# Performance work log

Measured on AMD Instinct MI355X. Metric: run time of the kernel, lower is better.

The kernel has to match this reference:

```python
import jax, jax.numpy as jnp
import numpy as np

B, S, D = 2, 2048, 1024
H = 16
HD = D // H  # 64


def setup_inputs() -> dict:
    key = jax.random.key(0)
    ks = jax.random.split(key, 6)
    sc = 1.0 / np.sqrt(D)
    x = jax.random.normal(ks[0], (B, S, D), dtype=jnp.float32)
    Wq = jax.random.normal(ks[1], (D, D), dtype=jnp.float32) * sc
    Wk = jax.random.normal(ks[2], (D, D), dtype=jnp.float32) * sc
    Wv = jax.random.normal(ks[3], (D, D), dtype=jnp.float32) * sc
    Wo = jax.random.normal(ks[4], (D, D), dtype=jnp.float32) * sc
    bo = jax.random.normal(ks[5], (D,), dtype=jnp.float32) * 0.01
    return {"x": x, "Wq": Wq, "Wk": Wk, "Wv": Wv, "Wo": Wo, "bo": bo}


def reference(x, Wq, Wk, Wv, Wo, bo):
    # projections: [B,S,D] -> [B,H,S,HD]
    def split_heads(t):
        return t.reshape(B, S, H, HD).transpose(0, 2, 1, 3)

    q = split_heads(x @ Wq)
    k = split_heads(x @ Wk)
    v = split_heads(x @ Wv)

    # naive full score matrix [B,H,S,S], masked causal, scaled softmax
    scores = jnp.einsum("bhqd,bhkd->bhqk", q, k)
    causal = jnp.tril(jnp.ones((S, S), dtype=bool))  # True = keep
    scores = jnp.where(causal, scores, -jnp.inf)
    attn = jax.nn.softmax(scores / np.sqrt(HD), axis=-1)

    ctx = jnp.einsum("bhqk,bhkd->bhqd", attn, v)  # [B,H,S,HD]
    ctx = ctx.transpose(0, 2, 1, 3).reshape(B, S, D)
    return ctx @ Wo + bo
```

## Files before the change

kernel.cpp:

```cpp
#include <hip/hip_runtime.h>

#define BB 2
#define SS 2048
#define DD 1024
#define HH 16
#define HD 64
#define MM (BB*SS)

typedef __bf16 bf16x8 __attribute__((ext_vector_type(8)));
typedef short  s16x4  __attribute__((ext_vector_type(4)));
typedef float  f32x4  __attribute__((ext_vector_type(4)));

#ifndef __has_builtin
#define __has_builtin(x) 0
#endif

__device__ __forceinline__ unsigned short f2bf(float f) {
    unsigned int u = __float_as_uint(f);
    u = (u + 0x7fffu + ((u >> 16) & 1u)) >> 16;
    return (unsigned short)u;
}
__device__ __forceinline__ unsigned int pack2(float a, float b) {
    return (unsigned int)f2bf(a) | ((unsigned int)f2bf(b) << 16);
}
__device__ __forceinline__ unsigned int pack2_fast(float a, float b) {
#if __has_builtin(__builtin_amdgcn_perm)
    return __builtin_amdgcn_perm(__float_as_uint(b) + 0x8000u,
                                 __float_as_uint(a) + 0x8000u, 0x07060302u);
#else
    return ((__float_as_uint(a) + 0x8000u) >> 16) |
           ((__float_as_uint(b) + 0x8000u) & 0xffff0000u);
#endif
}

__device__ __forceinline__ void gload_lds16(const unsigned short* g, unsigned short* l) {
    __builtin_amdgcn_global_load_lds(
        (const __attribute__((address_space(1))) void*)g,
        (__attribute__((address_space(3))) void*)l, 16, 0, 0);
}

__global__ __launch_bounds__(256) void cast_x_kernel(const float* __restrict__ x,
                                                     unsigned short* __restrict__ Xb) {
    int gid = blockIdx.x * 256 + threadIdx.x;
    int i = gid * 8;
    float4 a = *(const float4*)(x + i);
    float4 b = *(const float4*)(x + i + 4);
    uint4 o;
    o.x = pack2(a.x, a.y); o.y = pack2(a.z, a.w);
    o.z = pack2(b.x, b.y); o.w = pack2(b.z, b.w);
    ((uint4*)Xb)[gid] = o;
}

__global__ __launch_bounds__(256) void prep_w_kernel(const float* __restrict__ Wq,
                                                     const float* __restrict__ Wk,
                                                     const float* __restrict__ Wv,
                                                     const float* __restrict__ Wo,
                                                     unsigned short* __restrict__ Wqkvt,
                                                     unsigned short* __restrict__ Wot) {
    __shared__ float tile[32][33];
    int p = blockIdx.z;
    const float* src = (p == 0) ? Wq : (p == 1) ? Wk : (p == 2) ? Wv : Wo;
    unsigned short* dst = (p == 3) ? Wot : (Wqkvt + (size_t)p * DD * DD);
    int tx = threadIdx.x, ty = threadIdx.y;
    int n = blockIdx.x * 32 + tx;
#pragma unroll
    for (int i = 0; i < 4; ++i) {
        int k = blockIdx.y * 32 + ty + i * 8;
        tile[ty + i * 8][tx] = src[k * DD + n];
    }
    __syncthreads();
#pragma unroll
    for (int i = 0; i < 4; ++i) {
        int n2 = blockIdx.x * 32 + ty + i * 8;
        int k2 = blockIdx.y * 32 + tx;
        dst[n2 * DD + k2] = f2bf(tile[tx][ty + i * 8]);
    }
}

#define GEMM_K_LOOP(Aglob, Bglob)                                                 \
    __shared__ unsigned short smem[128 * 132];                                    \
    unsigned short (*As)[64]  = (unsigned short(*)[64])smem;                      \
    unsigned short (*Bs)[64]  = (unsigned short(*)[64])(smem + 128 * 64);         \
    unsigned short (*Es)[132] = (unsigned short(*)[132])smem;                     \
    const int n0 = blockIdx.x * 128, m0 = blockIdx.y * 128;                       \
    const int t = threadIdx.x;                                                    \
    const int wave = t >> 6, lane = t & 63;                                       \
    const int wm = wave >> 1, wn = wave & 1;                                      \
    const int l15 = lane & 15, quad = lane >> 4;                                  \
    const int lr = lane >> 3, lc = (lane & 7) * 8;                                \
    f32x4 acc[4][4];                                                              \
    _Pragma("unroll") for (int i = 0; i < 4; ++i)                                 \
        _Pragma("unroll") for (int j = 0; j < 4; ++j) acc[i][j] = f32x4{0,0,0,0}; \
    for (int kt = 0; kt < 16; ++kt) {                                             \
        if (kt) __syncthreads();                                                  \
        _Pragma("unroll") for (int i = 0; i < 4; ++i) {                           \
            int row = wave * 32 + i * 8;                                          \
            gload_lds16(Aglob + (size_t)(m0 + row + lr) * DD + kt * 64 + lc, &As[row][0]); \
            gload_lds16(Bglob + (size_t)(n0 + row + lr) * DD + kt * 64 + lc, &Bs[row][0]); \
        }                                                                         \
        __syncthreads();                                                          \
        _Pragma("unroll") for (int kh = 0; kh < 2; ++kh) {                        \
            bf16x8 af[4], bfr[4];                                                 \
            _Pragma("unroll") for (int s = 0; s < 4; ++s)                         \
                af[s] = *(const bf16x8*)&As[wm * 64 + s * 16 + l15][kh * 32 + quad * 8]; \
            _Pragma("unroll") for (int s = 0; s < 4; ++s)                         \
                bfr[s] = *(const bf16x8*)&Bs[wn * 64 + s * 16 + l15][kh * 32 + quad * 8]; \
            _Pragma("unroll") for (int i = 0; i < 4; ++i)                         \
                _Pragma("unroll") for (int j = 0; j < 4; ++j)                     \
                    acc[i][j] = __builtin_amdgcn_mfma_f32_16x16x32_bf16(af[i], bfr[j], acc[i][j], 0, 0, 0); \
        }                                                                         \
    }                                                                             \
    __syncthreads();

__global__ __launch_bounds__(256) void qkv_gemm_kernel(const unsigned short* __restrict__ Xb,
                                                       const unsigned short* __restrict__ Wt,
                                                       unsigned short* __restrict__ Qg,
                                                       unsigned short* __restrict__ Kg,
                                                       unsigned short* __restrict__ Vt) {
    GEMM_K_LOOP(Xb, Wt)
    const int p = n0 >> 10;
    const float qs = (p == 0) ? 0.18033688011112042f : 1.0f;
    if (p < 2) {
#pragma unroll
        for (int sm = 0; sm < 4; ++sm)
#pragma unroll
            for (int sn = 0; sn < 4; ++sn)
#pragma unroll
                for (int i = 0; i < 4; ++i)
                    Es[wm * 64 + sm * 16 + quad * 4 + i][wn * 64 + sn * 16 + l15] = f2bf(acc[sm][sn][i] * qs);
    } else {
#pragma unroll
        for (int sm = 0; sm < 4; ++sm)
#pragma unroll
            for (int sn = 0; sn < 4; ++sn)
#pragma unroll
                for (int i = 0; i < 4; ++i)
                    Es[wn * 64 + sn * 16 + l15][wm * 64 + sm * 16 + quad * 4 + i] = f2bf(acc[sm][sn][i]);
    }
    __syncthreads();
    const int h0 = (n0 & 1023) >> 6;
    if (p < 2) {
        unsigned short* dst0 = p ? Kg : Qg;
        int ml = t >> 1, seg = t & 1;
        int gm = m0 + ml, b = gm >> 11, s = gm & 2047;
        unsigned short* dptr = dst0 + ((size_t)(b * HH + h0 + seg) * SS + s) * HD;
#pragma unroll
        for (int j = 0; j < 8; ++j)
            *(uint4*)(dptr + j * 8) = *(const uint4*)&Es[ml][seg * 64 + j * 8];
    } else {
        int nl = t >> 1, mh = t & 1;
        int h = h0 + (nl >> 6), hd = nl & 63;
        int b = m0 >> 11, s0 = (m0 & 2047) + mh * 64;
        unsigned short* dptr = Vt + ((size_t)(b * HH + h) * HD + hd) * SS + s0;
#pragma unroll
        for (int j = 0; j < 8; ++j)
            *(uint4*)(dptr + j * 8) = *(const uint4*)&Es[nl][mh * 64 + j * 8];
    }
}

__global__ __launch_bounds__(256) void out_gemm_kernel(const unsigned short* __restrict__ Ctxb,
                                                       const unsigned short* __restrict__ Wot,
                                                       const float* __restrict__ bo,
                                                       float* __restrict__ out) {
    GEMM_K_LOOP(Ctxb, Wot)
    (void)Es;
#pragma unroll
    for (int sn = 0; sn < 4; ++sn) {
        int gn = n0 + wn * 64 + sn * 16 + l15;
        float bias = bo[gn];
#pragma unroll
        for (int sm = 0; sm < 4; ++sm)
#pragma unroll
            for (int i = 0; i < 4; ++i) {
                int gm = m0 + wm * 64 + sm * 16 + quad * 4 + i;
                out[(size_t)gm * DD + gn] = acc[sm][sn][i] + bias;
            }
    }
}

__global__ __launch_bounds__(256) void attn_kernel(const unsigned short* __restrict__ Qg,
                                                   const unsigned short* __restrict__ Kg,
                                                   const unsigned short* __restrict__ Vt,
                                                   unsigned short* __restrict__ Ctxb) {
    __shared__ unsigned short Ks[2][64][64];
    __shared__ unsigned short Vs[2][64][64];

    const int bh = blockIdx.x;
    const int qt = (int)gridDim.y - 1 - (int)blockIdx.y;
    const int t = threadIdx.x;
    const int wave = t >> 6, lane = t & 63;
    const int l15 = lane & 15, quad = lane >> 4;
    const int q0 = qt * 64;
    const int b = bh >> 4, h = bh & 15;

    const unsigned short* Qb = Qg + (size_t)bh * SS * HD;
    const unsigned short* Kb = Kg + (size_t)bh * SS * HD;
    const unsigned short* Vb = Vt + (size_t)bh * HD * SS;

    const int qrow = q0 + wave * 16 + l15;
    bf16x8 bq[2];
#pragma unroll
    for (int hh = 0; hh < 2; ++hh)
        bq[hh] = *(const bf16x8*)(Qb + (size_t)qrow * HD + hh * 32 + quad * 8);

    const int rloc = lane >> 3, pcl = lane & 7;
    const int csw = pcl ^ rloc;
    const unsigned short* ksrc[2];
    const unsigned short* vsrc[2];
#pragma unroll
    for (int j = 0; j < 2; ++j) {
        int row = (wave * 2 + j) * 8 + rloc;
        ksrc[j] = Kb + (size_t)row * HD + csw * 8;
        vsrc[j] = Vb + (size_t)row * SS + csw * 8;
    }

    f32x4 acc[4] = {f32x4{0,0,0,0}, f32x4{0,0,0,0}, f32x4{0,0,0,0}, f32x4{0,0,0,0}};
    float l = 0.f;
    const int nkt = qt + 1;

#pragma unroll
    for (int j = 0; j < 2; ++j) {
        gload_lds16(ksrc[j], &Ks[0][(wave * 2 + j) * 8][0]);
        gload_lds16(vsrc[j], &Vs[0][(wave * 2 + j) * 8][0]);
    }
    __syncthreads();

    for (int kt = 0; kt < nkt; ++kt) {
        const int buf = kt & 1;
        const int k0 = kt * 64;
        if (kt + 1 < nkt) {
            const int nb = buf ^ 1;
#pragma unroll
            for (int j = 0; j < 2; ++j) {
                gload_lds16(ksrc[j] + (size_t)(kt + 1) * 4096, &Ks[nb][(wave * 2 + j) * 8][0]);
                gload_lds16(vsrc[j] + (kt + 1) * 64,           &Vs[nb][(wave * 2 + j) * 8][0]);
            }
        }

        f32x4 St[4] = {f32x4{0,0,0,0}, f32x4{0,0,0,0}, f32x4{0,0,0,0}, f32x4{0,0,0,0}};
#pragma unroll
        for (int hh = 0; hh < 2; ++hh) {
            const int pcK = (hh * 4 + quad) ^ (l15 & 7);
            bf16x8 ak[4];
#pragma unroll
            for (int kb = 0; kb < 4; ++kb)
                ak[kb] = *(const bf16x8*)&Ks[buf][0][(kb * 16 + l15) * 64 + pcK * 8];
#pragma unroll
            for (int kb = 0; kb < 4; ++kb)
                St[kb] = __builtin_amdgcn_mfma_f32_16x16x32_bf16(ak[kb], bq[hh], St[kb], 0, 0, 0);
        }

        if (kt == qt) {
#pragma unroll
            for (int kb = 0; kb < 4; ++kb)
#pragma unroll
                for (int r = 0; r < 4; ++r)
                    if (k0 + kb * 16 + quad * 4 + r > qrow) St[kb][r] = -1e30f;
        }

        float lt = 0.f;
        s16x4 ap[4];
#pragma unroll
        for (int kb = 0; kb < 4; ++kb) {
            float e0 = __builtin_amdgcn_exp2f(St[kb][0]);
            float e1 = __builtin_amdgcn_exp2f(St[kb][1]);
            float e2 = __builtin_amdgcn_exp2f(St[kb][2]);
            float e3 = __builtin_amdgcn_exp2f(St[kb][3]);
            lt += (e0 + e1) + (e2 + e3);
            uint2 uu;
            uu.x = pack2_fast(e0, e1);
            uu.y = pack2_fast(e2, e3);
            ap[kb] = *(s16x4*)&uu;
        }
        lt += __shfl_xor(lt, 16, 64);
        lt += __shfl_xor(lt, 32, 64);
        l += lt;

#pragma unroll
        for (int kb = 0; kb < 4; ++kb) {
            s16x4 bv[4];
#pragma unroll
            for (int db = 0; db < 4; ++db) {
                const int pcV = (2 * kb + (quad >> 1)) ^ (l15 & 7);
                bv[db] = *(const s16x4*)&Vs[buf][0][(db * 16 + l15) * 64 + pcV * 8 + (quad & 1) * 4];
            }
#pragma unroll
            for (int db = 0; db < 4; ++db)
                acc[db] = __builtin_amdgcn_mfma_f32_16x16x16bf16_1k(ap[kb], bv[db], acc[db], 0, 0, 0);
        }

        if (kt + 1 < nkt) __syncthreads();
    }

    float linv = 1.0f / l;
#pragma unroll
    for (int r = 0; r < 4; ++r) {
        float ir = __shfl(linv, quad * 4 + r, 64);
        int gq = q0 + wave * 16 + quad * 4 + r;
        size_t base = ((size_t)(b * SS + gq)) * DD + h * HD;
#pragma unroll
        for (int db = 0; db < 4; ++db)
            Ctxb[base + db * 16 + l15] = f2bf(acc[db][r] * ir);
    }
}

extern "C" void kernel_launch(void* const* d_in, const int* in_sizes, int n_in,
                              void* d_out, int out_size, void* d_ws, size_t ws_size,
                              hipStream_t stream) {
    const float* x  = (const float*)d_in[0];
    const float* Wq = (const float*)d_in[1];
    const float* Wk = (const float*)d_in[2];
    const float* Wv = (const float*)d_in[3];
    const float* Wo = (const float*)d_in[4];
    const float* bo = (const float*)d_in[5];
    float* out = (float*)d_out;

    char* w = (char*)d_ws;
    unsigned short* Xb    = (unsigned short*)(w);
    unsigned short* Wqkvt = (unsigned short*)(w + (size_t)(8 << 20));
    unsigned short* Wot   = (unsigned short*)(w + (size_t)(14 << 20));
    unsigned short* Qg    = (unsigned short*)(w + (size_t)(16 << 20));
    unsigned short* Kg    = (unsigned short*)(w + (size_t)(24 << 20));
    unsigned short* Vt    = (unsigned short*)(w + (size_t)(32 << 20));
    unsigned short* Ctxb  = (unsigned short*)(w + (size_t)(40 << 20));

    cast_x_kernel<<<MM * DD / (256 * 8), 256, 0, stream>>>(x, Xb);
    prep_w_kernel<<<dim3(DD / 32, DD / 32, 4), dim3(32, 8), 0, stream>>>(Wq, Wk, Wv, Wo, Wqkvt, Wot);
    qkv_gemm_kernel<<<dim3(3 * DD / 128, MM / 128), 256, 0, stream>>>(Xb, Wqkvt, Qg, Kg, Vt);
    attn_kernel<<<dim3(BB * HH, SS / 64), 256, 0, stream>>>(Qg, Kg, Vt, Ctxb);
    out_gemm_kernel<<<dim3(DD / 128, MM / 128), 256, 0, stream>>>(Ctxb, Wot, bo, out);
}
```

Baseline: 186.5 us.

## Merge prep kernels and use 128-wide KV tiles in causal attention

Merges the x cast and weight transpose kernels into one launch that picks its job from the block index. The attention kernel now loads 128 keys per iteration (double-buffered K and V tiles in LDS with a new XOR swizzle) and processes them in 16-key chunks, skipping fully masked chunks on the final tile. The row-sum shuffle reduction moves out of the loop to the end. The goal is fewer barriers and loop iterations and one less kernel launch, at the cost of doubled LDS use, which may lower occupancy.

```diff
diff --git a/kernel.cpp b/kernel.cpp
--- a/kernel.cpp
+++ b/kernel.cpp
@@ -39,40 +39,45 @@
         (__attribute__((address_space(3))) void*)l, 16, 0, 0);
 }
 
-__global__ __launch_bounds__(256) void cast_x_kernel(const float* __restrict__ x,
-                                                     unsigned short* __restrict__ Xb) {
-    int gid = blockIdx.x * 256 + threadIdx.x;
-    int i = gid * 8;
-    float4 a = *(const float4*)(x + i);
-    float4 b = *(const float4*)(x + i + 4);
-    uint4 o;
-    o.x = pack2(a.x, a.y); o.y = pack2(a.z, a.w);
-    o.z = pack2(b.x, b.y); o.w = pack2(b.z, b.w);
-    ((uint4*)Xb)[gid] = o;
-}
-
-__global__ __launch_bounds__(256) void prep_w_kernel(const float* __restrict__ Wq,
-                                                     const float* __restrict__ Wk,
-                                                     const float* __restrict__ Wv,
-                                                     const float* __restrict__ Wo,
-                                                     unsigned short* __restrict__ Wqkvt,
-                                                     unsigned short* __restrict__ Wot) {
+__global__ __launch_bounds__(256) void prep_kernel(const float* __restrict__ x,
+                                                   const float* __restrict__ Wq,
+                                                   const float* __restrict__ Wk,
+                                                   const float* __restrict__ Wv,
+                                                   const float* __restrict__ Wo,
+                                                   unsigned short* __restrict__ Xb,
+                                                   unsigned short* __restrict__ Wqkvt,
+                                                   unsigned short* __restrict__ Wot) {
     __shared__ float tile[32][33];
-    int p = blockIdx.z;
+    const int bx = blockIdx.x;
+    const int t = threadIdx.x;
+    if (bx < 2048) {
+        int gid = bx * 256 + t;
+        int i = gid * 8;
+        float4 a = *(const float4*)(x + i);
+        float4 b = *(const float4*)(x + i + 4);
+        uint4 o;
+        o.x = pack2(a.x, a.y); o.y = pack2(a.z, a.w);
+        o.z = pack2(b.x, b.y); o.w = pack2(b.z, b.w);
+        ((uint4*)Xb)[gid] = o;
+        return;
+    }
+    int pb = bx - 2048;
+    int p = pb >> 10, rem = pb & 1023;
+    int bxx = rem & 31, byy = rem >> 5;
     const float* src = (p == 0) ? Wq : (p == 1) ? Wk : (p == 2) ? Wv : Wo;
     unsigned short* dst = (p == 3) ? Wot : (Wqkvt + (size_t)p * DD * DD);
-    int tx = threadIdx.x, ty = threadIdx.y;
-    int n = blockIdx.x * 32 + tx;
+    int tx = t & 31, ty = t >> 5;
+    int n = bxx * 32 + tx;
 #pragma unroll
     for (int i = 0; i < 4; ++i) {
-        int k = blockIdx.y * 32 + ty + i * 8;
+        int k = byy * 32 + ty + i * 8;
         tile[ty + i * 8][tx] = src[k * DD + n];
     }
     __syncthreads();
 #pragma unroll
     for (int i = 0; i < 4; ++i) {
-        int n2 = blockIdx.x * 32 + ty + i * 8;
-        int k2 = blockIdx.y * 32 + tx;
+        int n2 = bxx * 32 + ty + i * 8;
+        int k2 = byy * 32 + tx;
         dst[n2 * DD + k2] = f2bf(tile[tx][ty + i * 8]);
     }
 }
@@ -182,8 +187,8 @@
                                                    const unsigned short* __restrict__ Kg,
                                                    const unsigned short* __restrict__ Vt,
                                                    unsigned short* __restrict__ Ctxb) {
-    __shared__ unsigned short Ks[2][64][64];
-    __shared__ unsigned short Vs[2][64][64];
+    __shared__ unsigned short Ks[2][128][64];
+    __shared__ unsigned short Vs[2][64][128];
 
     const int bh = blockIdx.x;
     const int qt = (int)gridDim.y - 1 - (int)blockIdx.y;
@@ -191,6 +196,7 @@
     const int wave = t >> 6, lane = t & 63;
     const int l15 = lane & 15, quad = lane >> 4;
     const int q0 = qt * 64;
+    const int qmax = q0 + 63;
     const int b = bh >> 4, h = bh & 15;
 
     const unsigned short* Qb = Qg + (size_t)bh * SS * HD;
@@ -204,94 +210,80 @@
         bq[hh] = *(const bf16x8*)(Qb + (size_t)qrow * HD + hh * 32 + quad * 8);
 
     const int rloc = lane >> 3, pcl = lane & 7;
-    const int csw = pcl ^ rloc;
-    const unsigned short* ksrc[2];
-    const unsigned short* vsrc[2];
-#pragma unroll
-    for (int j = 0; j < 2; ++j) {
-        int row = (wave * 2 + j) * 8 + rloc;
-        ksrc[j] = Kb + (size_t)row * HD + csw * 8;
-        vsrc[j] = Vb + (size_t)row * SS + csw * 8;
+    const int vrl = lane >> 4, vgc = lane & 15;
+    const unsigned short* ksrc[4];
+    const unsigned short* vsrc[4];
+#pragma unroll
+    for (int j = 0; j < 4; ++j) {
+        int krow = (wave * 4 + j) * 8 + rloc;
+        ksrc[j] = Kb + (size_t)krow * HD + (pcl ^ rloc) * 8;
+        int vrow = wave * 16 + j * 4 + vrl;
+        vsrc[j] = Vb + (size_t)vrow * SS + (vgc ^ (vrow & 15)) * 8;
     }
 
     f32x4 acc[4] = {f32x4{0,0,0,0}, f32x4{0,0,0,0}, f32x4{0,0,0,0}, f32x4{0,0,0,0}};
     float l = 0.f;
-    const int nkt = qt + 1;
-
-#pragma unroll
-    for (int j = 0; j < 2; ++j) {
-        gload_lds16(ksrc[j], &Ks[0][(wave * 2 + j) * 8][0]);
-        gload_lds16(vsrc[j], &Vs[0][(wave * 2 + j) * 8][0]);
+    const int nkt = (qmax >> 7) + 1;
+
+#pragma unroll
+    for (int j = 0; j < 4; ++j) {
+        gload_lds16(ksrc[j], &Ks[0][(wave * 4 + j) * 8][0]);
+        gload_lds16(vsrc[j], &Vs[0][wave * 16 + j * 4][0]);
     }
     __syncthreads();
 
     for (int kt = 0; kt < nkt; ++kt) {
         const int buf = kt & 1;
-        const int k0 = kt * 64;
+        const int k0 = kt * 128;
         if (kt + 1 < nkt) {
             const int nb = buf ^ 1;
 #pragma unroll
-            for (int j = 0; j < 2; ++j) {
-                gload_lds16(ksrc[j] + (size_t)(kt + 1) * 4096, &Ks[nb][(wave * 2 + j) * 8][0]);
-                gload_lds16(vsrc[j] + (kt + 1) * 64,           &Vs[nb][(wave * 2 + j) * 8][0]);
+            for (int j = 0; j < 4; ++j) {
+                gload_lds16(ksrc[j] + (size_t)(kt + 1) * 128 * HD, &Ks[nb][(wave * 4 + j) * 8][0]);
+                gload_lds16(vsrc[j] + (kt + 1) * 128,              &Vs[nb][wave * 16 + j * 4][0]);
             }
         }
 
-        f32x4 St[4] = {f32x4{0,0,0,0}, f32x4{0,0,0,0}, f32x4{0,0,0,0}, f32x4{0,0,0,0}};
-#pragma unroll
-        for (int hh = 0; hh < 2; ++hh) {
-            const int pcK = (hh * 4 + quad) ^ (l15 & 7);
-            bf16x8 ak[4];
-#pragma unroll
-            for (int kb = 0; kb < 4; ++kb)
-                ak[kb] = *(const bf16x8*)&Ks[buf][0][(kb * 16 + l15) * 64 + pcK * 8];
-#pragma unroll
-            for (int kb = 0; kb < 4; ++kb)
-                St[kb] = __builtin_amdgcn_mfma_f32_16x16x32_bf16(ak[kb], bq[hh], St[kb], 0, 0, 0);
-        }
-
-        if (kt == qt) {
-#pragma unroll
-            for (int kb = 0; kb < 4; ++kb)
-#pragma unroll
-                for (int r = 0; r < 4; ++r)
-                    if (k0 + kb * 16 + quad * 4 + r > qrow) St[kb][r] = -1e30f;
-        }
-
-        float lt = 0.f;
-        s16x4 ap[4];
-#pragma unroll
-        for (int kb = 0; kb < 4; ++kb) {
-            float e0 = __builtin_amdgcn_exp2f(St[kb][0]);
-            float e1 = __builtin_amdgcn_exp2f(St[kb][1]);
-            float e2 = __builtin_amdgcn_exp2f(St[kb][2]);
-            float e3 = __builtin_amdgcn_exp2f(St[kb][3]);
-            lt += (e0 + e1) + (e2 + e3);
-            uint2 uu;
-            uu.x = pack2_fast(e0, e1);
-            uu.y = pack2_fast(e2, e3);
-            ap[kb] = *(s16x4*)&uu;
-        }
-        lt += __shfl_xor(lt, 16, 64);
-        lt += __shfl_xor(lt, 32, 64);
-        l += lt;
-
-#pragma unroll
-        for (int kb = 0; kb < 4; ++kb) {
-            s16x4 bv[4];
-#pragma unroll
-            for (int db = 0; db < 4; ++db) {
-                const int pcV = (2 * kb + (quad >> 1)) ^ (l15 & 7);
-                bv[db] = *(const s16x4*)&Vs[buf][0][(db * 16 + l15) * 64 + pcV * 8 + (quad & 1) * 4];
+        auto tile_body = [&](int kbmax, bool tail) {
+#pragma unroll
+            for (int kb = 0; kb < 8; ++kb) {
+                if (kb >= kbmax) continue;
+                f32x4 St = f32x4{0, 0, 0, 0};
+#pragma unroll
+                for (int hh = 0; hh < 2; ++hh) {
+                    bf16x8 ak = *(const bf16x8*)&Ks[buf][kb * 16 + l15][((hh * 4 + quad) ^ (l15 & 7)) * 8];
+                    St = __builtin_amdgcn_mfma_f32_16x16x32_bf16(ak, bq[hh], St, 0, 0, 0);
+                }
+                if (tail) {
+#pragma unroll
+                    for (int r = 0; r < 4; ++r)
+                        if (k0 + kb * 16 + quad * 4 + r > qrow) St[r] = -1e30f;
+                }
+                float e0 = __builtin_amdgcn_exp2f(St[0]);
+                float e1 = __builtin_amdgcn_exp2f(St[1]);
+                float e2 = __builtin_amdgcn_exp2f(St[2]);
+                float e3 = __builtin_amdgcn_exp2f(St[3]);
+                l += (e0 + e1) + (e2 + e3);
+                uint2 uu;
+                uu.x = pack2_fast(e0, e1);
+                uu.y = pack2_fast(e2, e3);
+                s16x4 ap = *(s16x4*)&uu;
+#pragma unroll
+                for (int db = 0; db < 4; ++db) {
+                    const int pg = (2 * kb + (quad >> 1)) ^ l15;
+                    s16x4 bv = *(const s16x4*)&Vs[buf][db * 16 + l15][pg * 8 + (quad & 1) * 4];
+                    acc[db] = __builtin_amdgcn_mfma_f32_16x16x16bf16_1k(ap, bv, acc[db], 0, 0, 0);
+                }
             }
-#pragma unroll
-            for (int db = 0; db < 4; ++db)
-                acc[db] = __builtin_amdgcn_mfma_f32_16x16x16bf16_1k(ap[kb], bv[db], acc[db], 0, 0, 0);
-        }
-
-        if (kt + 1 < nkt) __syncthreads();
-    }
-
+        };
+        if (kt == nkt - 1) tile_body(((qmax - k0) >> 4) + 1, true);
+        else               tile_body(8, false);
+
+        __syncthreads();
+    }
+
+    l += __shfl_xor(l, 16, 64);
+    l += __shfl_xor(l, 32, 64);
     float linv = 1.0f / l;
 #pragma unroll
     for (int r = 0; r < 4; ++r) {
@@ -324,8 +316,7 @@
     unsigned short* Vt    = (unsigned short*)(w + (size_t)(32 << 20));
     unsigned short* Ctxb  = (unsigned short*)(w + (size_t)(40 << 20));
 
-    cast_x_kernel<<<MM * DD / (256 * 8), 256, 0, stream>>>(x, Xb);
-    prep_w_kernel<<<dim3(DD / 32, DD / 32, 4), dim3(32, 8), 0, stream>>>(Wq, Wk, Wv, Wo, Wqkvt, Wot);
+    prep_kernel<<<6144, 256, 0, stream>>>(x, Wq, Wk, Wv, Wo, Xb, Wqkvt, Wot);
     qkv_gemm_kernel<<<dim3(3 * DD / 128, MM / 128), 256, 0, stream>>>(Xb, Wqkvt, Qg, Kg, Vt);
     attn_kernel<<<dim3(BB * HH, SS / 64), 256, 0, stream>>>(Qg, Kg, Vt, Ctxb);
     out_gemm_kernel<<<dim3(DD / 128, MM / 128), 256, 0, stream>>>(Ctxb, Wot, bo, out);
```

Result: faster. 180.3 us (-3.3%).
